# Kernel tuning notes

Hardware: AMD Instinct MI355X
Metric: run time of the kernel (lower is better)

The kernel has to match this reference:

```python
import jax, jax.numpy as jnp
import numpy as np

B, T, C, H = 4, 4096, 1024, 128

def setup_inputs() -> dict:
    key = jax.random.key(0)
    k1, k2, k3, k4 = jax.random.split(key, 4)
    ix = jax.random.normal(k1, (B, T, C), dtype=jnp.float32)
    Wq = jax.random.normal(k2, (C, H), dtype=jnp.float32) * (C ** -0.5)
    Wk = jax.random.normal(k3, (C, H), dtype=jnp.float32) * (C ** -0.5)
    Wv = jax.random.normal(k4, (C, H), dtype=jnp.float32) * (C ** -0.5)
    return {"ix": ix, "Wq": Wq, "Wk": Wk, "Wv": Wv}

def reference(ix, Wq, Wk, Wv):
    Bc, Tc, Cc = ix.shape
    q = ix @ Wq                      # [B,T,H]
    k = ix @ Wk                      # [B,T,H]
    v = ix @ Wv                      # [B,T,H]
    # NOTE: original computes k @ q^T (row index from k, col index from q),
    # scaled by n_embed**-0.5 (C, not head_size).
    wei = jnp.einsum('bth,bsh->bts', k, q) * (Cc ** -0.5)  # [B,T,T]
    causal = jnp.tril(jnp.ones((Tc, Tc), dtype=bool))
    wei = jnp.where(causal[None, :, :], wei, -jnp.inf)
    wei = jax.nn.softmax(wei, axis=-1)
    # dropout is identity in eval mode
    out = jnp.einsum('bts,bsh->bth', wei, v)  # [B,T,H]
    return out
```

## Files before the change

kernel.cpp:

```cpp
#include <hip/hip_runtime.h>
#include <hip/hip_bf16.h>

typedef __bf16 bf16x8 __attribute__((ext_vector_type(8)));
typedef float f32x4 __attribute__((ext_vector_type(4)));
typedef float f32x16 __attribute__((ext_vector_type(16)));
typedef unsigned u32x4 __attribute__((ext_vector_type(4)));
#define MFMA16 __builtin_amdgcn_mfma_f32_16x16x32_bf16
#define MFMA32 __builtin_amdgcn_mfma_f32_32x32x16_bf16

static constexpr int Bsz = 4, T = 4096, C = 1024, H = 128;
static constexpr int BT = Bsz * T;

__device__ __forceinline__ void gl2lds16(const __bf16* g, __bf16* l) {
    __builtin_amdgcn_global_load_lds(
        (const __attribute__((address_space(1))) void*)g,
        (__attribute__((address_space(3))) void*)l, 16, 0, 0);
}

__device__ __forceinline__ unsigned pk2(float a, float b) {
    unsigned short ua = __builtin_bit_cast(unsigned short, (__bf16)a);
    unsigned short ub = __builtin_bit_cast(unsigned short, (__bf16)b);
    return (unsigned)ua | ((unsigned)ub << 16);
}

__global__ __launch_bounds__(256) void k_wprep(
    const float* __restrict__ Wq, const float* __restrict__ Wk,
    const float* __restrict__ Wv, __bf16* __restrict__ WTall)
{
    int idx = blockIdx.x * 256 + threadIdx.x;
    int n = idx >> 10, k = idx & 1023;
    int mat = n >> 7, col = n & 127;
    const float* W = mat == 0 ? Wq : (mat == 1 ? Wk : Wv);
    float s = (mat == 1) ? 0.045084220f : 1.0f;
    WTall[idx] = (__bf16)(W[k * H + col] * s);
}

__global__ __launch_bounds__(512) void k_proj(
    const float* __restrict__ X, const __bf16* __restrict__ WTall,
    __bf16* __restrict__ Qp, __bf16* __restrict__ Kp, __bf16* __restrict__ VT)
{
    union Smem {
        struct { __bf16 a[2][64 * 64]; __bf16 b[2][192 * 64]; } s;
        __bf16 vt_e[128][72];
    };
    __shared__ Smem su;

    const int tid = threadIdx.x;
    const int lane = tid & 63, w = tid >> 6;
    const int c = lane & 15, hi = lane >> 4;
    const int wm = w >> 2, wn = w & 3;
    const int ny = blockIdx.x >> 8;
    const int m0 = (blockIdx.x & 255) * 64;
    const int xorv = (c & 7) << 3;

    const int arow = tid >> 3, ac8 = tid & 7;
    const float* aSrc = X + (size_t)(m0 + arow) * C + ac8 * 8;
    const int aDst = arow * 64 + ((ac8 * 8) ^ ((arow & 7) << 3));
    const int brl = lane >> 3, bch = lane & 7;
    const __bf16* Wbase = WTall + (size_t)ny * 192 * 1024;

    f32x4 acc[2][3];
    #pragma unroll
    for (int i = 0; i < 2; ++i)
        #pragma unroll
        for (int j = 0; j < 3; ++j) acc[i][j] = (f32x4){0.f, 0.f, 0.f, 0.f};

    #pragma unroll
    for (int ib = 0; ib < 3; ++ib) {
        int row = w * 24 + ib * 8 + brl;
        int ch = bch ^ (row & 7);
        gl2lds16(Wbase + (size_t)row * 1024 + ch * 8, &su.s.b[0][(w * 3 + ib) * 512]);
    }
    {
        float4 f0 = *(const float4*)aSrc;
        float4 f1 = *(const float4*)(aSrc + 4);
        bf16x8 av;
        av[0] = (__bf16)f0.x; av[1] = (__bf16)f0.y; av[2] = (__bf16)f0.z; av[3] = (__bf16)f0.w;
        av[4] = (__bf16)f1.x; av[5] = (__bf16)f1.y; av[6] = (__bf16)f1.z; av[7] = (__bf16)f1.w;
        *(bf16x8*)&su.s.a[0][aDst] = av;
    }
    __syncthreads();

    for (int t = 0; t < 16; ++t) {
        int cur = t & 1;
        float4 g0, g1;
        if (t < 15) {
            int k0 = (t + 1) * 64;
            #pragma unroll
            for (int ib = 0; ib < 3; ++ib) {
                int row = w * 24 + ib * 8 + brl;
                int ch = bch ^ (row & 7);
                gl2lds16(Wbase + (size_t)row * 1024 + k0 + ch * 8,
                         &su.s.b[cur ^ 1][(w * 3 + ib) * 512]);
            }
            g0 = *(const float4*)(aSrc + k0);
            g1 = *(const float4*)(aSrc + k0 + 4);
        }
        #pragma unroll
        for (int kk = 0; kk < 2; ++kk) {
            bf16x8 a0 = *(const bf16x8*)&su.s.a[cur][(wm * 32 + c) * 64 + ((kk * 32 + hi * 8) ^ xorv)];
            bf16x8 a1 = *(const bf16x8*)&su.s.a[cur][(wm * 32 + 16 + c) * 64 + ((kk * 32 + hi * 8) ^ xorv)];
            #pragma unroll
            for (int fn = 0; fn < 3; ++fn) {
                bf16x8 bb = *(const bf16x8*)&su.s.b[cur][(wn * 48 + fn * 16 + c) * 64 + ((kk * 32 + hi * 8) ^ xorv)];
                acc[0][fn] = MFMA16(a0, bb, acc[0][fn], 0, 0, 0);
                acc[1][fn] = MFMA16(a1, bb, acc[1][fn], 0, 0, 0);
            }
        }
        if (t < 15) {
            bf16x8 av;
            av[0] = (__bf16)g0.x; av[1] = (__bf16)g0.y; av[2] = (__bf16)g0.z; av[3] = (__bf16)g0.w;
            av[4] = (__bf16)g1.x; av[5] = (__bf16)g1.y; av[6] = (__bf16)g1.z; av[7] = (__bf16)g1.w;
            *(bf16x8*)&su.s.a[cur ^ 1][aDst] = av;
        }
        __syncthreads();
    }

    #pragma unroll
    for (int mi = 0; mi < 2; ++mi) {
        int rowl = wm * 32 + mi * 16 + hi * 4;
        #pragma unroll
        for (int fn = 0; fn < 3; ++fn) {
            int nb = ny * 192 + wn * 48 + fn * 16;
            int mat = nb >> 7, colb = (nb & 127) + c;
            #pragma unroll
            for (int r = 0; r < 4; ++r) {
                __bf16 v = (__bf16)acc[mi][fn][r];
                if (mat == 0)      Qp[(size_t)(m0 + rowl + r) * H + colb] = v;
                else if (mat == 1) Kp[(size_t)(m0 + rowl + r) * H + colb] = v;
                else               su.vt_e[colb][rowl + r] = v;
            }
        }
    }
    __syncthreads();
    if (ny == 1) {
        int d = tid >> 2, tc = (tid & 3) * 16;
        int b = m0 >> 12, tl = m0 & (T - 1);
        __bf16* dst = VT + ((size_t)b * H + d) * T + tl + tc;
        const __bf16* s2 = &su.vt_e[d][tc];
        *(uint4*)dst = *(const uint4*)s2;
        *(uint4*)(dst + 8) = *(const uint4*)(s2 + 8);
    }
}

__global__ __launch_bounds__(256) void k_attn(
    const __bf16* __restrict__ Ka, const __bf16* __restrict__ Qb,
    const __bf16* __restrict__ VT, float* __restrict__ Out,
    float* __restrict__ Po, float* __restrict__ Pl)
{
    __shared__ float oacc[64][132];
    __shared__ float sml[4][32];

    const int tid = threadIdx.x, lane = tid & 63, w = tid >> 6;
    const int t31 = lane & 31, hi5 = lane >> 5;
    const int wm = w >> 1, ws = w & 1;

    const int bi = blockIdx.x;
    const int p = bi & 1, b = (bi >> 1) & 3, u = bi >> 3;

    const __bf16* Kb  = Ka + (size_t)b * T * H;
    const __bf16* Qbb = Qb + (size_t)b * T * H;
    const __bf16* Vb  = VT + (size_t)b * H * T;

    #pragma unroll 1
    for (int half = 0; half < 2; ++half) {
        const int j  = half ? (63 - u) : u;
        const int t0 = j * 64;
        const int nsteps = j + 1;
        const int rbase = t0 + wm * 32;
        const int tg = rbase + t31;

        bf16x8 kb[8];
        #pragma unroll
        for (int kc = 0; kc < 8; ++kc)
            kb[kc] = *(const bf16x8*)(Kb + (size_t)(rbase + t31) * H + kc * 16 + hi5 * 8);

        f32x16 oc[4];
        #pragma unroll
        for (int dn = 0; dn < 4; ++dn)
            #pragma unroll
            for (int r = 0; r < 16; ++r) oc[dn][r] = 0.f;
        float ol = 0.f;

        for (int i = p; i < nsteps; i += 2) {
            const int sbase = i * 64 + ws * 32;
            bf16x8 qa[8];
            #pragma unroll
            for (int kc = 0; kc < 8; ++kc)
                qa[kc] = *(const bf16x8*)(Qbb + (size_t)(sbase + t31) * H + kc * 16 + hi5 * 8);
            bf16x8 vb[4][2];
            #pragma unroll
            for (int dn = 0; dn < 4; ++dn)
                #pragma unroll
                for (int ks = 0; ks < 2; ++ks)
                    vb[dn][ks] = *(const bf16x8*)(Vb + (size_t)(dn * 32 + t31) * T + sbase + ks * 16 + hi5 * 8);

            f32x16 accA, accB;
            #pragma unroll
            for (int r = 0; r < 16; ++r) { accA[r] = 0.f; accB[r] = 0.f; }
            #pragma unroll
            for (int kc = 0; kc < 4; ++kc) accA = MFMA32(qa[kc], kb[kc], accA, 0, 0, 0);
            #pragma unroll
            for (int kc = 4; kc < 8; ++kc) accB = MFMA32(qa[kc], kb[kc], accB, 0, 0, 0);

            const bool dz = (sbase + 31 >= rbase);
            float pv[16];
            #pragma unroll
            for (int r = 0; r < 16; ++r) {
                float e = __builtin_amdgcn_exp2f(accA[r] + accB[r]);
                if (dz) {
                    int sg = sbase + (r & 3) + 8 * (r >> 2) + 4 * hi5;
                    if (sg > tg) e = 0.f;
                }
                pv[r] = e;
            }
            float rs = ((pv[0] + pv[1]) + (pv[2] + pv[3])) + ((pv[4] + pv[5]) + (pv[6] + pv[7]))
                     + ((pv[8] + pv[9]) + (pv[10] + pv[11])) + ((pv[12] + pv[13]) + (pv[14] + pv[15]));
            ol += rs;

            unsigned x1 = pk2(pv[0], pv[1]),  x2 = pk2(pv[2], pv[3]);
            unsigned y1 = pk2(pv[4], pv[5]),  y2 = pk2(pv[6], pv[7]);
            unsigned x3 = pk2(pv[8], pv[9]),  x4 = pk2(pv[10], pv[11]);
            unsigned y3 = pk2(pv[12], pv[13]), y4 = pk2(pv[14], pv[15]);
            unsigned sx1 = __shfl_xor((int)x1, 32), sx2 = __shfl_xor((int)x2, 32);
            unsigned sy1 = __shfl_xor((int)y1, 32), sy2 = __shfl_xor((int)y2, 32);
            unsigned sx3 = __shfl_xor((int)x3, 32), sx4 = __shfl_xor((int)x4, 32);
            unsigned sy3 = __shfl_xor((int)y3, 32), sy4 = __shfl_xor((int)y4, 32);
            u32x4 wA, wB;
            wA[0] = hi5 ? sy1 : x1;  wA[1] = hi5 ? sy2 : x2;
            wA[2] = hi5 ? y1 : sx1;  wA[3] = hi5 ? y2 : sx2;
            wB[0] = hi5 ? sy3 : x3;  wB[1] = hi5 ? sy4 : x4;
            wB[2] = hi5 ? y3 : sx3;  wB[3] = hi5 ? y4 : sx4;
            bf16x8 paA = __builtin_bit_cast(bf16x8, wA);
            bf16x8 paB = __builtin_bit_cast(bf16x8, wB);

            #pragma unroll
            for (int dn = 0; dn < 4; ++dn) {
                oc[dn] = MFMA32(paA, vb[dn][0], oc[dn], 0, 0, 0);
                oc[dn] = MFMA32(paB, vb[dn][1], oc[dn], 0, 0, 0);
            }
        }

        ol += __shfl_xor(ol, 32);
        if (lane < 32) sml[w][lane] = ol;

        if (ws == 0) {
            #pragma unroll
            for (int dn = 0; dn < 4; ++dn)
                #pragma unroll
                for (int r = 0; r < 16; ++r) {
                    int row = wm * 32 + (r & 3) + 8 * (r >> 2) + 4 * hi5;
                    oacc[row][dn * 32 + t31] = oc[dn][r];
                }
        }
        __syncthreads();
        if (ws == 1) {
            #pragma unroll
            for (int dn = 0; dn < 4; ++dn)
                #pragma unroll
                for (int r = 0; r < 16; ++r) {
                    int row = wm * 32 + (r & 3) + 8 * (r >> 2) + 4 * hi5;
                    oacc[row][dn * 32 + t31] += oc[dn][r];
                }
        }
        __syncthreads();
        {
            int row = tid >> 2, cq = (tid & 3) * 4;
            float L = sml[(row >> 5) * 2][row & 31] + sml[(row >> 5) * 2 + 1][row & 31];
            float* dst = (p == 0 ? Out : Po) + ((size_t)b * T + t0 + row) * H;
            #pragma unroll
            for (int k = 0; k < 8; ++k) {
                int col = cq + k * 16;
                float4 v;
                v.x = oacc[row][col];
                v.y = oacc[row][col + 1];
                v.z = oacc[row][col + 2];
                v.w = oacc[row][col + 3];
                *(float4*)(dst + col) = v;
            }
            if ((tid & 3) == 0) Pl[(size_t)p * BT + b * T + t0 + row] = L;
        }
        __syncthreads();
    }
}

__global__ __launch_bounds__(256) void k_merge(
    float* __restrict__ Out, const float* __restrict__ Po,
    const float* __restrict__ Pl)
{
    size_t idx = ((size_t)blockIdx.x * 256 + threadIdx.x) * 8;
    size_t row = idx >> 7;
    float inv = 1.0f / (Pl[row] + Pl[BT + row]);
    float4 a0 = *(const float4*)(Out + idx);
    float4 a1 = *(const float4*)(Out + idx + 4);
    float4 p0 = *(const float4*)(Po + idx);
    float4 p1 = *(const float4*)(Po + idx + 4);
    float4 r0, r1;
    r0.x = (a0.x + p0.x) * inv; r0.y = (a0.y + p0.y) * inv;
    r0.z = (a0.z + p0.z) * inv; r0.w = (a0.w + p0.w) * inv;
    r1.x = (a1.x + p1.x) * inv; r1.y = (a1.y + p1.y) * inv;
    r1.z = (a1.z + p1.z) * inv; r1.w = (a1.w + p1.w) * inv;
    *(float4*)(Out + idx)     = r0;
    *(float4*)(Out + idx + 4) = r1;
}

extern "C" void kernel_launch(void* const* d_in, const int* in_sizes, int n_in,
                              void* d_out, int out_size, void* d_ws, size_t ws_size,
                              hipStream_t stream) {
    const float* ix = (const float*)d_in[0];
    const float* Wq = (const float*)d_in[1];
    const float* Wk = (const float*)d_in[2];
    const float* Wv = (const float*)d_in[3];
    float* out = (float*)d_out;

    __bf16* WTall = (__bf16*)d_ws;
    __bf16* Qp = WTall + 393216;
    __bf16* Kp = Qp + (size_t)BT * H;
    __bf16* VT = Kp + (size_t)BT * H;
    float*  Po = (float*)(VT + (size_t)BT * H);
    float*  Pl = Po + (size_t)BT * H;

    k_wprep<<<dim3(1536), 256, 0, stream>>>(Wq, Wk, Wv, WTall);
    k_proj<<<dim3(512), 512, 0, stream>>>(ix, WTall, Qp, Kp, VT);
    k_attn<<<dim3(256), 256, 0, stream>>>(Kp, Qp, VT, out, Po, Pl);
    k_merge<<<dim3(1024), 256, 0, stream>>>(out, Po, Pl);
}
```

Measured before the change: 106.7 us.

## Split key range across 8 warps in-block and drop separate merge kernel

The attention kernel now runs 512 threads per block. Each block owns a 32-row query tile, and its 8 warps split the key steps (2 sub-tiles × 4 strided partitions). Partial outputs are reduced in LDS through four serialized accumulation rounds and normalized in-kernel. This removes the split across two blocks, the partial-output/rowsum workspace writes, and the separate merge kernel launch with its global read-modify-write pass. The cost is more barriers and a serialized LDS reduction per tile, plus K fragments loaded per 32-row tile instead of per 64-row tile.

```diff
diff --git a/kernel.cpp b/kernel.cpp
--- a/kernel.cpp
+++ b/kernel.cpp
@@ -143,20 +143,20 @@
     }
 }
 
-__global__ __launch_bounds__(256) void k_attn(
+__global__ __launch_bounds__(512) void k_attn(
     const __bf16* __restrict__ Ka, const __bf16* __restrict__ Qb,
-    const __bf16* __restrict__ VT, float* __restrict__ Out,
-    float* __restrict__ Po, float* __restrict__ Pl)
+    const __bf16* __restrict__ VT, float* __restrict__ Out)
 {
-    __shared__ float oacc[64][132];
-    __shared__ float sml[4][32];
+    __shared__ float oaccA[32][132];
+    __shared__ float oaccB[32][132];
+    __shared__ float sml[8][32];
 
     const int tid = threadIdx.x, lane = tid & 63, w = tid >> 6;
     const int t31 = lane & 31, hi5 = lane >> 5;
-    const int wm = w >> 1, ws = w & 1;
+    const int ws = w >> 2, sp = w & 3;
 
     const int bi = blockIdx.x;
-    const int p = bi & 1, b = (bi >> 1) & 3, u = bi >> 3;
+    const int b = bi & 3, vpr = bi >> 2;
 
     const __bf16* Kb  = Ka + (size_t)b * T * H;
     const __bf16* Qbb = Qb + (size_t)b * T * H;
@@ -164,16 +164,15 @@
 
     #pragma unroll 1
     for (int half = 0; half < 2; ++half) {
-        const int j  = half ? (63 - u) : u;
-        const int t0 = j * 64;
-        const int nsteps = j + 1;
-        const int rbase = t0 + wm * 32;
-        const int tg = rbase + t31;
+        const int v  = half ? (127 - vpr) : vpr;
+        const int t0 = v * 32;
+        const int nsteps = (v >> 1) + 1;
+        const int tg = t0 + t31;
 
         bf16x8 kb[8];
         #pragma unroll
         for (int kc = 0; kc < 8; ++kc)
-            kb[kc] = *(const bf16x8*)(Kb + (size_t)(rbase + t31) * H + kc * 16 + hi5 * 8);
+            kb[kc] = *(const bf16x8*)(Kb + (size_t)(t0 + t31) * H + kc * 16 + hi5 * 8);
 
         f32x16 oc[4];
         #pragma unroll
@@ -182,7 +181,7 @@
             for (int r = 0; r < 16; ++r) oc[dn][r] = 0.f;
         float ol = 0.f;
 
-        for (int i = p; i < nsteps; i += 2) {
+        for (int i = sp; i < nsteps; i += 4) {
             const int sbase = i * 64 + ws * 32;
             bf16x8 qa[8];
             #pragma unroll
@@ -203,7 +202,7 @@
             #pragma unroll
             for (int kc = 4; kc < 8; ++kc) accB = MFMA32(qa[kc], kb[kc], accB, 0, 0, 0);
 
-            const bool dz = (sbase + 31 >= rbase);
+            const bool dz = (sbase + 31 >= t0);
             float pv[16];
             #pragma unroll
             for (int r = 0; r < 16; ++r) {
@@ -244,64 +243,42 @@
         ol += __shfl_xor(ol, 32);
         if (lane < 32) sml[w][lane] = ol;
 
-        if (ws == 0) {
-            #pragma unroll
-            for (int dn = 0; dn < 4; ++dn)
+        for (int g = 0; g < 4; ++g) {
+            __syncthreads();
+            if (sp == g) {
+                float* oa = (ws == 0) ? &oaccA[0][0] : &oaccB[0][0];
                 #pragma unroll
-                for (int r = 0; r < 16; ++r) {
-                    int row = wm * 32 + (r & 3) + 8 * (r >> 2) + 4 * hi5;
-                    oacc[row][dn * 32 + t31] = oc[dn][r];
-                }
-        }
-        __syncthreads();
-        if (ws == 1) {
-            #pragma unroll
-            for (int dn = 0; dn < 4; ++dn)
-                #pragma unroll
-                for (int r = 0; r < 16; ++r) {
-                    int row = wm * 32 + (r & 3) + 8 * (r >> 2) + 4 * hi5;
-                    oacc[row][dn * 32 + t31] += oc[dn][r];
-                }
+                for (int dn = 0; dn < 4; ++dn)
+                    #pragma unroll
+                    for (int r = 0; r < 16; ++r) {
+                        int row = (r & 3) + 8 * (r >> 2) + 4 * hi5;
+                        int col = dn * 32 + t31;
+                        if (g == 0) oa[row * 132 + col]  = oc[dn][r];
+                        else        oa[row * 132 + col] += oc[dn][r];
+                    }
+            }
         }
         __syncthreads();
         {
-            int row = tid >> 2, cq = (tid & 3) * 4;
-            float L = sml[(row >> 5) * 2][row & 31] + sml[(row >> 5) * 2 + 1][row & 31];
-            float* dst = (p == 0 ? Out : Po) + ((size_t)b * T + t0 + row) * H;
-            #pragma unroll
-            for (int k = 0; k < 8; ++k) {
-                int col = cq + k * 16;
-                float4 v;
-                v.x = oacc[row][col];
-                v.y = oacc[row][col + 1];
-                v.z = oacc[row][col + 2];
-                v.w = oacc[row][col + 3];
-                *(float4*)(dst + col) = v;
-            }
-            if ((tid & 3) == 0) Pl[(size_t)p * BT + b * T + t0 + row] = L;
+            int row = tid >> 4, col0 = (tid & 15) * 8;
+            float L = sml[0][row] + sml[1][row] + sml[2][row] + sml[3][row]
+                    + sml[4][row] + sml[5][row] + sml[6][row] + sml[7][row];
+            float inv = 1.0f / L;
+            float* dst = Out + ((size_t)b * T + t0 + row) * H + col0;
+            float4 v0, v1;
+            v0.x = (oaccA[row][col0]     + oaccB[row][col0])     * inv;
+            v0.y = (oaccA[row][col0 + 1] + oaccB[row][col0 + 1]) * inv;
+            v0.z = (oaccA[row][col0 + 2] + oaccB[row][col0 + 2]) * inv;
+            v0.w = (oaccA[row][col0 + 3] + oaccB[row][col0 + 3]) * inv;
+            v1.x = (oaccA[row][col0 + 4] + oaccB[row][col0 + 4]) * inv;
+            v1.y = (oaccA[row][col0 + 5] + oaccB[row][col0 + 5]) * inv;
+            v1.z = (oaccA[row][col0 + 6] + oaccB[row][col0 + 6]) * inv;
+            v1.w = (oaccA[row][col0 + 7] + oaccB[row][col0 + 7]) * inv;
+            *(float4*)dst       = v0;
+            *(float4*)(dst + 4) = v1;
         }
         __syncthreads();
     }
-}
-
-__global__ __launch_bounds__(256) void k_merge(
-    float* __restrict__ Out, const float* __restrict__ Po,
-    const float* __restrict__ Pl)
-{
-    size_t idx = ((size_t)blockIdx.x * 256 + threadIdx.x) * 8;
-    size_t row = idx >> 7;
-    float inv = 1.0f / (Pl[row] + Pl[BT + row]);
-    float4 a0 = *(const float4*)(Out + idx);
-    float4 a1 = *(const float4*)(Out + idx + 4);
-    float4 p0 = *(const float4*)(Po + idx);
-    float4 p1 = *(const float4*)(Po + idx + 4);
-    float4 r0, r1;
-    r0.x = (a0.x + p0.x) * inv; r0.y = (a0.y + p0.y) * inv;
-    r0.z = (a0.z + p0.z) * inv; r0.w = (a0.w + p0.w) * inv;
-    r1.x = (a1.x + p1.x) * inv; r1.y = (a1.y + p1.y) * inv;
-    r1.z = (a1.z + p1.z) * inv; r1.w = (a1.w + p1.w) * inv;
-    *(float4*)(Out + idx)     = r0;
-    *(float4*)(Out + idx + 4) = r1;
 }
 
 extern "C" void kernel_launch(void* const* d_in, const int* in_sizes, int n_in,
@@ -317,11 +294,8 @@
     __bf16* Qp = WTall + 393216;
     __bf16* Kp = Qp + (size_t)BT * H;
     __bf16* VT = Kp + (size_t)BT * H;
-    float*  Po = (float*)(VT + (size_t)BT * H);
-    float*  Pl = Po + (size_t)BT * H;
 
     k_wprep<<<dim3(1536), 256, 0, stream>>>(Wq, Wk, Wv, WTall);
     k_proj<<<dim3(512), 512, 0, stream>>>(ix, WTall, Qp, Kp, VT);
-    k_attn<<<dim3(256), 256, 0, stream>>>(Kp, Qp, VT, out, Po, Pl);
-    k_merge<<<dim3(1024), 256, 0, stream>>>(out, Po, Pl);
-}
+    k_attn<<<dim3(256), 512, 0, stream>>>(Kp, Qp, VT, out);
+}
```

Measured after the change: 106.0 us. Within noise of the previous version (-0.7%).

## Have each wave cover both query row tiles to reuse Q/V loads

Applied to the files above, without the earlier changes.

Each wave now holds K fragments for both 32-row halves of the 64-row tile. It processes a 32-column S slice against both, so every loaded Q and V fragment feeds two row tiles and per-wave global traffic is halved. Waves split the S loop four ways, and partial outputs are reduced in shared memory through four serialized accumulation phases. The cost is doubled accumulator registers (launch bounds forced to one block per SM-equivalent), more barriers, and a stride-4 loop that may unbalance work for short rows.

```diff
diff --git a/kernel.cpp b/kernel.cpp
--- a/kernel.cpp
+++ b/kernel.cpp
@@ -143,17 +143,17 @@
     }
 }
 
-__global__ __launch_bounds__(256) void k_attn(
+__global__ __launch_bounds__(256, 1) void k_attn(
     const __bf16* __restrict__ Ka, const __bf16* __restrict__ Qb,
     const __bf16* __restrict__ VT, float* __restrict__ Out,
     float* __restrict__ Po, float* __restrict__ Pl)
 {
     __shared__ float oacc[64][132];
-    __shared__ float sml[4][32];
+    __shared__ float sml[4][64];
 
     const int tid = threadIdx.x, lane = tid & 63, w = tid >> 6;
     const int t31 = lane & 31, hi5 = lane >> 5;
-    const int wm = w >> 1, ws = w & 1;
+    const int ws = w >> 1, sp = w & 1;
 
     const int bi = blockIdx.x;
     const int p = bi & 1, b = (bi >> 1) & 3, u = bi >> 3;
@@ -167,22 +167,24 @@
         const int j  = half ? (63 - u) : u;
         const int t0 = j * 64;
         const int nsteps = j + 1;
-        const int rbase = t0 + wm * 32;
-        const int tg = rbase + t31;
-
-        bf16x8 kb[8];
-        #pragma unroll
-        for (int kc = 0; kc < 8; ++kc)
-            kb[kc] = *(const bf16x8*)(Kb + (size_t)(rbase + t31) * H + kc * 16 + hi5 * 8);
-
-        f32x16 oc[4];
-        #pragma unroll
-        for (int dn = 0; dn < 4; ++dn)
-            #pragma unroll
-            for (int r = 0; r < 16; ++r) oc[dn][r] = 0.f;
-        float ol = 0.f;
-
-        for (int i = p; i < nsteps; i += 2) {
+
+        bf16x8 kb2[2][8];
+        #pragma unroll
+        for (int tt = 0; tt < 2; ++tt)
+            #pragma unroll
+            for (int kc = 0; kc < 8; ++kc)
+                kb2[tt][kc] = *(const bf16x8*)(Kb + (size_t)(t0 + tt * 32 + t31) * H + kc * 16 + hi5 * 8);
+
+        f32x16 oc[2][4];
+        #pragma unroll
+        for (int tt = 0; tt < 2; ++tt)
+            #pragma unroll
+            for (int dn = 0; dn < 4; ++dn)
+                #pragma unroll
+                for (int r = 0; r < 16; ++r) oc[tt][dn][r] = 0.f;
+        float ol0 = 0.f, ol1 = 0.f;
+
+        for (int i = p + 2 * sp; i < nsteps; i += 4) {
             const int sbase = i * 64 + ws * 32;
             bf16x8 qa[8];
             #pragma unroll
@@ -195,88 +197,89 @@
                 for (int ks = 0; ks < 2; ++ks)
                     vb[dn][ks] = *(const bf16x8*)(Vb + (size_t)(dn * 32 + t31) * T + sbase + ks * 16 + hi5 * 8);
 
-            f32x16 accA, accB;
-            #pragma unroll
-            for (int r = 0; r < 16; ++r) { accA[r] = 0.f; accB[r] = 0.f; }
-            #pragma unroll
-            for (int kc = 0; kc < 4; ++kc) accA = MFMA32(qa[kc], kb[kc], accA, 0, 0, 0);
-            #pragma unroll
-            for (int kc = 4; kc < 8; ++kc) accB = MFMA32(qa[kc], kb[kc], accB, 0, 0, 0);
-
-            const bool dz = (sbase + 31 >= rbase);
-            float pv[16];
-            #pragma unroll
-            for (int r = 0; r < 16; ++r) {
-                float e = __builtin_amdgcn_exp2f(accA[r] + accB[r]);
-                if (dz) {
-                    int sg = sbase + (r & 3) + 8 * (r >> 2) + 4 * hi5;
-                    if (sg > tg) e = 0.f;
+            #pragma unroll
+            for (int tt = 0; tt < 2; ++tt) {
+                const int tg = t0 + tt * 32 + t31;
+                f32x16 accA, accB;
+                #pragma unroll
+                for (int r = 0; r < 16; ++r) { accA[r] = 0.f; accB[r] = 0.f; }
+                #pragma unroll
+                for (int kc = 0; kc < 4; ++kc) accA = MFMA32(qa[kc], kb2[tt][kc], accA, 0, 0, 0);
+                #pragma unroll
+                for (int kc = 4; kc < 8; ++kc) accB = MFMA32(qa[kc], kb2[tt][kc], accB, 0, 0, 0);
+
+                const bool dz = (sbase + 31 >= t0 + tt * 32);
+                float pv[16];
+                #pragma unroll
+                for (int r = 0; r < 16; ++r) {
+                    float e = __builtin_amdgcn_exp2f(accA[r] + accB[r]);
+                    if (dz) {
+                        int sg = sbase + (r & 3) + 8 * (r >> 2) + 4 * hi5;
+                        if (sg > tg) e = 0.f;
+                    }
+                    pv[r] = e;
                 }
-                pv[r] = e;
-            }
-            float rs = ((pv[0] + pv[1]) + (pv[2] + pv[3])) + ((pv[4] + pv[5]) + (pv[6] + pv[7]))
-                     + ((pv[8] + pv[9]) + (pv[10] + pv[11])) + ((pv[12] + pv[13]) + (pv[14] + pv[15]));
-            ol += rs;
-
-            unsigned x1 = pk2(pv[0], pv[1]),  x2 = pk2(pv[2], pv[3]);
-            unsigned y1 = pk2(pv[4], pv[5]),  y2 = pk2(pv[6], pv[7]);
-            unsigned x3 = pk2(pv[8], pv[9]),  x4 = pk2(pv[10], pv[11]);
-            unsigned y3 = pk2(pv[12], pv[13]), y4 = pk2(pv[14], pv[15]);
-            unsigned sx1 = __shfl_xor((int)x1, 32), sx2 = __shfl_xor((int)x2, 32);
-            unsigned sy1 = __shfl_xor((int)y1, 32), sy2 = __shfl_xor((int)y2, 32);
-            unsigned sx3 = __shfl_xor((int)x3, 32), sx4 = __shfl_xor((int)x4, 32);
-            unsigned sy3 = __shfl_xor((int)y3, 32), sy4 = __shfl_xor((int)y4, 32);
-            u32x4 wA, wB;
-            wA[0] = hi5 ? sy1 : x1;  wA[1] = hi5 ? sy2 : x2;
-            wA[2] = hi5 ? y1 : sx1;  wA[3] = hi5 ? y2 : sx2;
-            wB[0] = hi5 ? sy3 : x3;  wB[1] = hi5 ? sy4 : x4;
-            wB[2] = hi5 ? y3 : sx3;  wB[3] = hi5 ? y4 : sx4;
-            bf16x8 paA = __builtin_bit_cast(bf16x8, wA);
-            bf16x8 paB = __builtin_bit_cast(bf16x8, wB);
-
-            #pragma unroll
-            for (int dn = 0; dn < 4; ++dn) {
-                oc[dn] = MFMA32(paA, vb[dn][0], oc[dn], 0, 0, 0);
-                oc[dn] = MFMA32(paB, vb[dn][1], oc[dn], 0, 0, 0);
-            }
-        }
-
-        ol += __shfl_xor(ol, 32);
-        if (lane < 32) sml[w][lane] = ol;
-
-        if (ws == 0) {
-            #pragma unroll
-            for (int dn = 0; dn < 4; ++dn)
-                #pragma unroll
-                for (int r = 0; r < 16; ++r) {
-                    int row = wm * 32 + (r & 3) + 8 * (r >> 2) + 4 * hi5;
-                    oacc[row][dn * 32 + t31] = oc[dn][r];
+                float rs = ((pv[0] + pv[1]) + (pv[2] + pv[3])) + ((pv[4] + pv[5]) + (pv[6] + pv[7]))
+                         + ((pv[8] + pv[9]) + (pv[10] + pv[11])) + ((pv[12] + pv[13]) + (pv[14] + pv[15]));
+                if (tt == 0) ol0 += rs; else ol1 += rs;
+
+                unsigned x1 = pk2(pv[0], pv[1]),  x2 = pk2(pv[2], pv[3]);
+                unsigned y1 = pk2(pv[4], pv[5]),  y2 = pk2(pv[6], pv[7]);
+                unsigned x3 = pk2(pv[8], pv[9]),  x4 = pk2(pv[10], pv[11]);
+                unsigned y3 = pk2(pv[12], pv[13]), y4 = pk2(pv[14], pv[15]);
+                unsigned sx1 = __shfl_xor((int)x1, 32), sx2 = __shfl_xor((int)x2, 32);
+                unsigned sy1 = __shfl_xor((int)y1, 32), sy2 = __shfl_xor((int)y2, 32);
+                unsigned sx3 = __shfl_xor((int)x3, 32), sx4 = __shfl_xor((int)x4, 32);
+                unsigned sy3 = __shfl_xor((int)y3, 32), sy4 = __shfl_xor((int)y4, 32);
+                u32x4 wA, wB;
+                wA[0] = hi5 ? sy1 : x1;  wA[1] = hi5 ? sy2 : x2;
+                wA[2] = hi5 ? y1 : sx1;  wA[3] = hi5 ? y2 : sx2;
+                wB[0] = hi5 ? sy3 : x3;  wB[1] = hi5 ? sy4 : x4;
+                wB[2] = hi5 ? y3 : sx3;  wB[3] = hi5 ? y4 : sx4;
+                bf16x8 paA = __builtin_bit_cast(bf16x8, wA);
+                bf16x8 paB = __builtin_bit_cast(bf16x8, wB);
+
+                #pragma unroll
+                for (int dn = 0; dn < 4; ++dn) {
+                    oc[tt][dn] = MFMA32(paA, vb[dn][0], oc[tt][dn], 0, 0, 0);
+                    oc[tt][dn] = MFMA32(paB, vb[dn][1], oc[tt][dn], 0, 0, 0);
                 }
-        }
-        __syncthreads();
-        if (ws == 1) {
-            #pragma unroll
-            for (int dn = 0; dn < 4; ++dn)
-                #pragma unroll
-                for (int r = 0; r < 16; ++r) {
-                    int row = wm * 32 + (r & 3) + 8 * (r >> 2) + 4 * hi5;
-                    oacc[row][dn * 32 + t31] += oc[dn][r];
-                }
+            }
+        }
+
+        ol0 += __shfl_xor(ol0, 32);
+        ol1 += __shfl_xor(ol1, 32);
+        if (lane < 32) { sml[w][t31] = ol0; sml[w][32 + t31] = ol1; }
+
+        for (int g = 0; g < 4; ++g) {
+            __syncthreads();
+            if (w == g) {
+                #pragma unroll
+                for (int tt = 0; tt < 2; ++tt)
+                    #pragma unroll
+                    for (int dn = 0; dn < 4; ++dn)
+                        #pragma unroll
+                        for (int r = 0; r < 16; ++r) {
+                            int row = tt * 32 + (r & 3) + 8 * (r >> 2) + 4 * hi5;
+                            int col = dn * 32 + t31;
+                            if (g == 0) oacc[row][col]  = oc[tt][dn][r];
+                            else        oacc[row][col] += oc[tt][dn][r];
+                        }
+            }
         }
         __syncthreads();
         {
-            int row = tid >> 2, cq = (tid & 3) * 4;
-            float L = sml[(row >> 5) * 2][row & 31] + sml[(row >> 5) * 2 + 1][row & 31];
-            float* dst = (p == 0 ? Out : Po) + ((size_t)b * T + t0 + row) * H;
-            #pragma unroll
-            for (int k = 0; k < 8; ++k) {
-                int col = cq + k * 16;
+            int row = tid >> 2, col0 = (tid & 3) * 32;
+            float L = sml[0][row] + sml[1][row] + sml[2][row] + sml[3][row];
+            float* dst = (p == 0 ? Out : Po) + ((size_t)b * T + t0 + row) * H + col0;
+            #pragma unroll
+            for (int k = 0; k < 32; k += 4) {
                 float4 v;
-                v.x = oacc[row][col];
-                v.y = oacc[row][col + 1];
-                v.z = oacc[row][col + 2];
-                v.w = oacc[row][col + 3];
-                *(float4*)(dst + col) = v;
+                v.x = oacc[row][col0 + k];
+                v.y = oacc[row][col0 + k + 1];
+                v.z = oacc[row][col0 + k + 2];
+                v.w = oacc[row][col0 + k + 3];
+                *(float4*)(dst + k) = v;
             }
             if ((tid & 3) == 0) Pl[(size_t)p * BT + b * T + t0 + row] = L;
         }
```

Measured after the change: 89.61 us. 1.19x faster.
